# Kernel optimization log

Hardware: AMD Instinct MI355X
Metric: run time of the kernel (lower is better)

Reference implementation:

```python
import jax, jax.numpy as jnp
import numpy as np

GELU_C = 0.7978845608028654  # sqrt(2/pi)

def new_gelu(x):
    return 0.5 * x * (1.0 + jnp.tanh(GELU_C * (x + 0.044715 * x ** 3)))

def signed_quant(x, num_non_signbits, max_value):
    n = 2 ** num_non_signbits
    return jnp.sign(x) * jnp.minimum(jnp.round(jnp.abs(x) / max_value * n) + 1.0, float(n - 1))

def reverse_signed_quant(q, num_non_signbits, max_value):
    n = 2 ** num_non_signbits
    return jnp.sign(q) * (jnp.abs(q) - 1.0) / n * max_value

def setup_inputs() -> dict:
    key = jax.random.key(0)
    k1, k2, k3 = jax.random.split(key, 3)
    B, S, NX, NF = 4, 2048, 1024, 4096
    inp = jax.random.normal(k1, (B, S, NX), dtype=jnp.float32)
    weight = jax.random.normal(k2, (NX, NF), dtype=jnp.float32) * 0.02
    bias = jnp.zeros((NF,), dtype=jnp.float32)
    return {"input": inp, "weight": weight, "bias": bias}

def reference(input, weight, bias):
    # idx = 0 -> threshold=0.0, num_bits_to_calculate=3, weight bits=3
    threshold = 0.0
    num_bits = 3
    w_bits = 3
    max_input_value = 8.0
    nx = weight.shape[0]
    # per-input-row power-of-two weight scale: [nx, 1]
    max_weight_value = 2.0 ** jnp.round(jnp.log2(jnp.max(jnp.abs(weight), axis=-1, keepdims=True)))
    in_q = signed_quant(input, num_bits, max_input_value)
    w_q = signed_quant(weight, w_bits, max_weight_value)
    b_q = signed_quant(bias, num_bits, max_input_value)
    # low-precision prediction scores
    out_sign = (in_q @ w_q) / nx / (2.0 ** ((num_bits + w_bits) / 2))
    # dequantized approximate output + GELU
    out_rev = (reverse_signed_quant(in_q, num_bits, max_input_value)
               @ reverse_signed_quant(w_q, w_bits, max_weight_value)
               + reverse_signed_quant(b_q, num_bits, max_input_value))
    gelu_rev = new_gelu(out_rev)
    # full-precision path
    full = new_gelu(input @ weight + bias)
    return jnp.where(out_sign < threshold, gelu_rev, full)
```

## Files before the change

### kernel.cpp

```cpp
#include <hip/hip_runtime.h>
#include <hip/hip_bf16.h>

#define M_DIM 8192
#define K_DIM 1024
#define N_DIM 4096
#define BUF_BYTES 32768

typedef __attribute__((ext_vector_type(8))) short bf16x8;
typedef __attribute__((ext_vector_type(4))) int i32x4;
typedef __attribute__((ext_vector_type(16))) int i32x16;
typedef __attribute__((ext_vector_type(16))) float f32x16;

__device__ __forceinline__ short f2bf(float f) {
  unsigned u = __builtin_bit_cast(unsigned, f);
  u = (u + 0x7fffu + ((u >> 16) & 1u)) >> 16;
  return (short)u;
}

__device__ __forceinline__ unsigned f2fp8(float v) {
  unsigned b = __builtin_bit_cast(unsigned, v);
  unsigned sg = (b >> 24) & 0x80u;
  unsigned ab = b & 0x7fffffffu;
  if (ab == 0) return sg;
  int e = (int)(ab >> 23) - 127;
  unsigned m3 = (ab >> 20) & 7u;
  if (e >= -6) return sg | (unsigned)((e + 7) << 3) | m3;
  return sg | ((8u + m3) >> (-6 - e));
}

__device__ __forceinline__ float gelu_f(float x) {
  float u = 0.7978845608028654f * (x + 0.044715f * x * x * x);
  float e = __expf(2.0f * u);
  float t = 1.0f - 2.0f / (e + 1.0f);
  return 0.5f * x * (1.0f + t);
}

__device__ __forceinline__ void gload16(const void* g, void* l) {
  __builtin_amdgcn_global_load_lds((const __attribute__((address_space(1))) void*)g,
                                   (__attribute__((address_space(3))) void*)l, 16, 0, 0);
}

__global__ void rowmax_kernel(const float* __restrict__ w, float* __restrict__ mw) {
  int row = blockIdx.x * 4 + (threadIdx.x >> 6);
  int lane = threadIdx.x & 63;
  const float4* rp = (const float4*)(w + (size_t)row * N_DIM);
  float m = 0.0f;
#pragma unroll
  for (int it = 0; it < 16; ++it) {
    float4 v = rp[it * 64 + lane];
    m = fmaxf(m, fmaxf(fmaxf(fabsf(v.x), fabsf(v.y)), fmaxf(fabsf(v.z), fabsf(v.w))));
  }
#pragma unroll
  for (int off = 32; off > 0; off >>= 1) m = fmaxf(m, __shfl_xor(m, off, 64));
  if (lane == 0) mw[row] = exp2f(rintf(log2f(m)));
}

__global__ void prep_a_kernel(const float* __restrict__ inp, signed char* __restrict__ aqi,
                              unsigned char* __restrict__ adf, short* __restrict__ af) {
  int c = blockIdx.x * 256 + threadIdx.x;
  int kg = c >> 13, m = c & 8191;
  const float4* src = (const float4*)(inp + (size_t)m * K_DIM + kg * 16);
  float xs[16];
#pragma unroll
  for (int v = 0; v < 4; ++v) {
    float4 t = src[v];
    xs[v * 4 + 0] = t.x; xs[v * 4 + 1] = t.y; xs[v * 4 + 2] = t.z; xs[v * 4 + 3] = t.w;
  }
  int qi[4] = {0, 0, 0, 0};
  unsigned long long f8lo = 0ull, f8hi = 0ull;
  bf16x8 b0, b1;
#pragma unroll
  for (int j = 0; j < 16; ++j) {
    float x = xs[j];
    float s = (x > 0.f) ? 1.f : ((x < 0.f) ? -1.f : 0.f);
    float r = rintf(fabsf(x));
    int iq = (int)(s * fminf(r + 1.f, 7.f));
    qi[j >> 2] |= (iq & 255) << ((j & 3) * 8);
    unsigned f8 = f2fp8(s * fminf(r, 6.f));
    if (j < 8) f8lo |= (unsigned long long)f8 << (j * 8);
    else       f8hi |= (unsigned long long)f8 << ((j - 8) * 8);
    short bb = f2bf(x);
    if (j < 8) b0[j] = bb; else b1[j - 8] = bb;
  }
  *(i32x4*)(aqi + ((size_t)kg * M_DIM + m) * 16) = (i32x4){qi[0], qi[1], qi[2], qi[3]};
  *(unsigned long long*)(adf + ((size_t)(2 * kg) * M_DIM + m) * 8) = f8lo;
  *(unsigned long long*)(adf + ((size_t)(2 * kg + 1) * M_DIM + m) * 8) = f8hi;
  *(bf16x8*)(af + ((size_t)(2 * kg) * M_DIM + m) * 8) = b0;
  *(bf16x8*)(af + ((size_t)(2 * kg + 1) * M_DIM + m) * 8) = b1;
}

__global__ void prep_w_kernel(const float* __restrict__ w, const float* __restrict__ mw,
                              signed char* __restrict__ wqi, unsigned char* __restrict__ wdf,
                              short* __restrict__ wf) {
  int c = blockIdx.x * 256 + threadIdx.x;
  int kg = c >> 12, n = c & 4095;
  int qi[4] = {0, 0, 0, 0};
  unsigned long long f8lo = 0ull, f8hi = 0ull;
  bf16x8 b0, b1;
#pragma unroll
  for (int j = 0; j < 16; ++j) {
    float wv = w[(size_t)(kg * 16 + j) * N_DIM + n];
    float sc = mw[kg * 16 + j];
    float s = (wv > 0.f) ? 1.f : ((wv < 0.f) ? -1.f : 0.f);
    float r = rintf(fabsf(wv) * (8.0f / sc));
    int iq = (int)(s * fminf(r + 1.f, 7.f));
    qi[j >> 2] |= (iq & 255) << ((j & 3) * 8);
    unsigned f8 = f2fp8(s * fminf(r, 6.f) * 0.125f * sc);
    if (j < 8) f8lo |= (unsigned long long)f8 << (j * 8);
    else       f8hi |= (unsigned long long)f8 << ((j - 8) * 8);
    short bb = f2bf(wv);
    if (j < 8) b0[j] = bb; else b1[j - 8] = bb;
  }
  *(i32x4*)(wqi + ((size_t)kg * N_DIM + n) * 16) = (i32x4){qi[0], qi[1], qi[2], qi[3]};
  *(unsigned long long*)(wdf + ((size_t)(2 * kg) * N_DIM + n) * 8) = f8lo;
  *(unsigned long long*)(wdf + ((size_t)(2 * kg + 1) * N_DIM + n) * 8) = f8hi;
  *(bf16x8*)(wf + ((size_t)(2 * kg) * N_DIM + n) * 8) = b0;
  *(bf16x8*)(wf + ((size_t)(2 * kg + 1) * N_DIM + n) * 8) = b1;
}

__global__ __launch_bounds__(256, 2) void fused_gemm_kernel(
    const signed char* __restrict__ aqi, const unsigned char* __restrict__ adf,
    const short* __restrict__ af, const signed char* __restrict__ wqi,
    const unsigned char* __restrict__ wdf, const short* __restrict__ wf,
    const float* __restrict__ bias, float* __restrict__ out) {
  extern __shared__ char lds[];

  const int tid = threadIdx.x;
  const int wid = tid >> 6;
  const int lane = tid & 63;

  int bid = blockIdx.x;
  bid = (bid & 7) * 256 + (bid >> 3);
  const int bm0 = (bid >> 5) * 128;
  const int bn0 = (bid & 31) * 128;

  const int wr = wid >> 1;
  const int wc = wid & 1;

  const char* gb[8]; int gs[8]; int lo[8];
#pragma unroll
  for (int i = 0; i < 8; ++i) {
    int u = wid * 8 + i;
    lo[i] = u * 1024 + lane * 16;
    if (u < 4) {
      int o = u * 64 + lane; int h2 = o >> 7, row = o & 127;
      gb[i] = (const char*)aqi + ((size_t)h2 * M_DIM + bm0 + row) * 16;
      gs[i] = 32 * M_DIM;
    } else if (u < 8) {
      int kg = u - 4;
      gb[i] = (const char*)adf + ((size_t)kg * M_DIM + bm0) * 8 + lane * 16;
      gs[i] = 32 * M_DIM;
    } else if (u < 16) {
      int o = (u - 8) * 64 + lane; int kg = o >> 7, row = o & 127;
      gb[i] = (const char*)af + ((size_t)kg * M_DIM + bm0 + row) * 16;
      gs[i] = 64 * M_DIM;
    } else if (u < 20) {
      int o = (u - 16) * 64 + lane; int h2 = o >> 7, col = o & 127;
      gb[i] = (const char*)wqi + ((size_t)h2 * N_DIM + bn0 + col) * 16;
      gs[i] = 32 * N_DIM;
    } else if (u < 24) {
      int kg = u - 20;
      gb[i] = (const char*)wdf + ((size_t)kg * N_DIM + bn0) * 8 + lane * 16;
      gs[i] = 32 * N_DIM;
    } else {
      int o = (u - 24) * 64 + lane; int kg = o >> 7, col = o & 127;
      gb[i] = (const char*)wf + ((size_t)kg * N_DIM + bn0 + col) * 16;
      gs[i] = 64 * N_DIM;
    }
  }

  const int h = lane >> 5;
  const int l31 = lane & 31;
  const int ra = wr * 64 + l31;
  const int rb = wc * 64 + l31;

  i32x16 acc0[2][2];
  f32x16 acc1[2][2], acc2[2][2];
  const i32x16 zi = {0, 0, 0, 0, 0, 0, 0, 0, 0, 0, 0, 0, 0, 0, 0, 0};
  const f32x16 zf = {0, 0, 0, 0, 0, 0, 0, 0, 0, 0, 0, 0, 0, 0, 0, 0};
#pragma unroll
  for (int mf = 0; mf < 2; ++mf)
#pragma unroll
    for (int nf = 0; nf < 2; ++nf) { acc0[mf][nf] = zi; acc1[mf][nf] = zf; acc2[mf][nf] = zf; }

#pragma unroll
  for (int i = 0; i < 8; ++i) gload16(gb[i], lds + lo[i]);

  for (int t = 0; t < 32; ++t) {
    const int cb = (t & 1) * BUF_BYTES;
    if (t < 31) {
      const int nb = ((t + 1) & 1) * BUF_BYTES;
#pragma unroll
      for (int i = 0; i < 8; ++i)
        gload16(gb[i] + (size_t)(t + 1) * gs[i], lds + nb + lo[i]);
      asm volatile("s_waitcnt vmcnt(8)" ::: "memory");
    } else {
      asm volatile("s_waitcnt vmcnt(0)" ::: "memory");
    }
    __builtin_amdgcn_s_barrier();
    __builtin_amdgcn_sched_barrier(0);

    const char* B = lds + cb;
    __builtin_amdgcn_s_setprio(1);
    {
      i32x4 a0[2], b0[2];
#pragma unroll
      for (int mf = 0; mf < 2; ++mf)
        a0[mf] = *(const i32x4*)(B + (h * 128 + ra + mf * 32) * 16);
#pragma unroll
      for (int nf = 0; nf < 2; ++nf)
        b0[nf] = *(const i32x4*)(B + 16384 + (h * 128 + rb + nf * 32) * 16);
#pragma unroll
      for (int mf = 0; mf < 2; ++mf)
#pragma unroll
        for (int nf = 0; nf < 2; ++nf)
          acc0[mf][nf] =
              __builtin_amdgcn_mfma_i32_32x32x32_i8(a0[mf], b0[nf], acc0[mf][nf], 0, 0, 0);
    }
#pragma unroll
    for (int kk = 0; kk < 2; ++kk) {
      long a1[2], b1[2];
#pragma unroll
      for (int mf = 0; mf < 2; ++mf)
        a1[mf] = *(const long*)(B + 4096 + ((kk * 2 + h) * 128 + ra + mf * 32) * 8);
#pragma unroll
      for (int nf = 0; nf < 2; ++nf)
        b1[nf] = *(const long*)(B + 20480 + ((kk * 2 + h) * 128 + rb + nf * 32) * 8);
#pragma unroll
      for (int mf = 0; mf < 2; ++mf)
#pragma unroll
        for (int nf = 0; nf < 2; ++nf)
          acc1[mf][nf] = __builtin_amdgcn_mfma_f32_32x32x16_fp8_fp8(a1[mf], b1[nf],
                                                                    acc1[mf][nf], 0, 0, 0);
    }
#pragma unroll
    for (int kk = 0; kk < 2; ++kk) {
      bf16x8 a2[2], b2[2];
#pragma unroll
      for (int mf = 0; mf < 2; ++mf)
        a2[mf] = *(const bf16x8*)(B + 8192 + ((kk * 2 + h) * 128 + ra + mf * 32) * 16);
#pragma unroll
      for (int nf = 0; nf < 2; ++nf)
        b2[nf] = *(const bf16x8*)(B + 24576 + ((kk * 2 + h) * 128 + rb + nf * 32) * 16);
#pragma unroll
      for (int mf = 0; mf < 2; ++mf)
#pragma unroll
        for (int nf = 0; nf < 2; ++nf)
          acc2[mf][nf] = __builtin_amdgcn_mfma_f32_32x32x16_bf16(a2[mf], b2[nf],
                                                                 acc2[mf][nf], 0, 0, 0);
    }
    __builtin_amdgcn_s_setprio(0);
    asm volatile("s_waitcnt lgkmcnt(0)" ::: "memory");
    __builtin_amdgcn_sched_barrier(0);
    __builtin_amdgcn_s_barrier();
  }

#pragma unroll
  for (int nf = 0; nf < 2; ++nf) {
    const int col = bn0 + rb + nf * 32;
    const float bv = bias[col];
    const float sb = (bv > 0.f) ? 1.f : ((bv < 0.f) ? -1.f : 0.f);
    const float db = sb * fminf(rintf(fabsf(bv)), 6.f);
#pragma unroll
    for (int mf = 0; mf < 2; ++mf) {
#pragma unroll
      for (int r = 0; r < 16; ++r) {
        const int row = bm0 + wr * 64 + mf * 32 + (r & 3) + 8 * (r >> 2) + 4 * h;
        float x = (acc0[mf][nf][r] < 0) ? (acc1[mf][nf][r] + db) : (acc2[mf][nf][r] + bv);
        out[(size_t)row * N_DIM + col] = gelu_f(x);
      }
    }
  }
}

extern "C" void kernel_launch(void* const* d_in, const int* in_sizes, int n_in,
                              void* d_out, int out_size, void* d_ws, size_t ws_size,
                              hipStream_t stream) {
  const float* inp = (const float*)d_in[0];
  const float* w = (const float*)d_in[1];
  const float* bias = (const float*)d_in[2];
  float* out = (float*)d_out;

  char* p = (char*)d_ws;
  short* af = (short*)p;             p += (size_t)M_DIM * K_DIM * 2;
  short* wf = (short*)p;             p += (size_t)K_DIM * N_DIM * 2;
  signed char* aqi = (signed char*)p; p += (size_t)M_DIM * K_DIM;
  unsigned char* adf = (unsigned char*)p; p += (size_t)M_DIM * K_DIM;
  signed char* wqi = (signed char*)p; p += (size_t)K_DIM * N_DIM;
  unsigned char* wdf = (unsigned char*)p; p += (size_t)K_DIM * N_DIM;
  float* mw = (float*)p;

  const int lds_bytes = 2 * BUF_BYTES;
  hipFuncSetAttribute((const void*)fused_gemm_kernel,
                      hipFuncAttributeMaxDynamicSharedMemorySize, lds_bytes);

  rowmax_kernel<<<K_DIM / 4, 256, 0, stream>>>(w, mw);
  prep_a_kernel<<<(M_DIM * K_DIM / 16) / 256, 256, 0, stream>>>(inp, aqi, adf, af);
  prep_w_kernel<<<(K_DIM * N_DIM / 16) / 256, 256, 0, stream>>>(w, mw, wqi, wdf, wf);
  fused_gemm_kernel<<<(M_DIM / 128) * (N_DIM / 128), 256, lds_bytes, stream>>>(
      aqi, adf, af, wqi, wdf, wf, bias, out);
}
```

Measured before the change: 213.0 us.

## Reshape GEMM tiles to 256x64, stream weight fragments directly into registers

Changes the block tile from 128x128 to 256x64, with each of four waves owning 64 rows across all 64 columns. Only the activation operands are staged through LDS, with dedicated waves loading each stream. The weight fragments (int8, fp8, bf16) are loaded straight from global memory into registers, and the vmcnt waits are adjusted to match. The XCD-aware block mapping is rewritten for the new grid. The aim is to halve LDS traffic and drop the weight LDS reads, at the cost of uncoalesced, unshared global weight loads and lower reuse of the weight operand.

```diff
diff --git a/kernel.cpp b/kernel.cpp
--- a/kernel.cpp
+++ b/kernel.cpp
@@ -126,53 +126,18 @@
   extern __shared__ char lds[];
 
   const int tid = threadIdx.x;
-  const int wid = tid >> 6;
+  const int wid_s = __builtin_amdgcn_readfirstlane(tid >> 6);
   const int lane = tid & 63;
 
-  int bid = blockIdx.x;
-  bid = (bid & 7) * 256 + (bid >> 3);
-  const int bm0 = (bid >> 5) * 128;
-  const int bn0 = (bid & 31) * 128;
-
-  const int wr = wid >> 1;
-  const int wc = wid & 1;
-
-  const char* gb[8]; int gs[8]; int lo[8];
-#pragma unroll
-  for (int i = 0; i < 8; ++i) {
-    int u = wid * 8 + i;
-    lo[i] = u * 1024 + lane * 16;
-    if (u < 4) {
-      int o = u * 64 + lane; int h2 = o >> 7, row = o & 127;
-      gb[i] = (const char*)aqi + ((size_t)h2 * M_DIM + bm0 + row) * 16;
-      gs[i] = 32 * M_DIM;
-    } else if (u < 8) {
-      int kg = u - 4;
-      gb[i] = (const char*)adf + ((size_t)kg * M_DIM + bm0) * 8 + lane * 16;
-      gs[i] = 32 * M_DIM;
-    } else if (u < 16) {
-      int o = (u - 8) * 64 + lane; int kg = o >> 7, row = o & 127;
-      gb[i] = (const char*)af + ((size_t)kg * M_DIM + bm0 + row) * 16;
-      gs[i] = 64 * M_DIM;
-    } else if (u < 20) {
-      int o = (u - 16) * 64 + lane; int h2 = o >> 7, col = o & 127;
-      gb[i] = (const char*)wqi + ((size_t)h2 * N_DIM + bn0 + col) * 16;
-      gs[i] = 32 * N_DIM;
-    } else if (u < 24) {
-      int kg = u - 20;
-      gb[i] = (const char*)wdf + ((size_t)kg * N_DIM + bn0) * 8 + lane * 16;
-      gs[i] = 32 * N_DIM;
-    } else {
-      int o = (u - 24) * 64 + lane; int kg = o >> 7, col = o & 127;
-      gb[i] = (const char*)wf + ((size_t)kg * N_DIM + bn0 + col) * 16;
-      gs[i] = 64 * N_DIM;
-    }
-  }
+  int raw = blockIdx.x;
+  int xcd = raw & 7, local = raw >> 3;
+  const int bm0 = ((xcd >> 2) * 16 + (local >> 4)) * 256;
+  const int bn0 = ((xcd & 3) * 16 + (local & 15)) * 64;
 
   const int h = lane >> 5;
   const int l31 = lane & 31;
-  const int ra = wr * 64 + l31;
-  const int rb = wc * 64 + l31;
+  const int ra = wid_s * 64 + l31;
+  const int cb = bn0 + l31;
 
   i32x16 acc0[2][2];
   f32x16 acc1[2][2], acc2[2][2];
@@ -183,33 +148,72 @@
 #pragma unroll
     for (int nf = 0; nf < 2; ++nf) { acc0[mf][nf] = zi; acc1[mf][nf] = zf; acc2[mf][nf] = zf; }
 
-#pragma unroll
-  for (int i = 0; i < 8; ++i) gload16(gb[i], lds + lo[i]);
-
+  auto stage = [&](int t, char* buf) {
+    if (wid_s == 0) {
+#pragma unroll
+      for (int i = 0; i < 8; ++i)
+        gload16((const char*)aqi +
+                    ((size_t)(2 * t + (i >> 2)) * M_DIM + bm0 + (i & 3) * 64 + lane) * 16,
+                buf + i * 1024 + lane * 16);
+    } else if (wid_s == 1) {
+#pragma unroll
+      for (int i = 0; i < 8; ++i)
+        gload16((const char*)adf + ((size_t)(4 * t + (i >> 1)) * M_DIM + bm0 + (i & 1) * 128) * 8 +
+                    lane * 16,
+                buf + (8 + i) * 1024 + lane * 16);
+    } else {
+#pragma unroll
+      for (int i = 0; i < 8; ++i) {
+        int j = (wid_s - 2) * 8 + i;
+        gload16((const char*)af +
+                    ((size_t)(4 * t + (j >> 2)) * M_DIM + bm0 + (j & 3) * 64 + lane) * 16,
+                buf + (16 + j) * 1024 + lane * 16);
+      }
+    }
+  };
+
+  const char* pq0 = (const char*)wqi + ((size_t)h * N_DIM + cb) * 16;
+  const char* pq1 = (const char*)wdf + ((size_t)h * N_DIM + cb) * 8;
+  const char* pq2 = (const char*)wf + ((size_t)h * N_DIM + cb) * 16;
+  const size_t sq0 = (size_t)2 * N_DIM * 16;
+  const size_t sq1 = (size_t)4 * N_DIM * 8;
+  const size_t sq2 = (size_t)4 * N_DIM * 16;
+  const size_t kq1 = (size_t)2 * N_DIM * 8;
+  const size_t kq2 = (size_t)2 * N_DIM * 16;
+
+  stage(0, lds);
+
+#pragma unroll 1
   for (int t = 0; t < 32; ++t) {
-    const int cb = (t & 1) * BUF_BYTES;
-    if (t < 31) {
-      const int nb = ((t + 1) & 1) * BUF_BYTES;
-#pragma unroll
-      for (int i = 0; i < 8; ++i)
-        gload16(gb[i] + (size_t)(t + 1) * gs[i], lds + nb + lo[i]);
-      asm volatile("s_waitcnt vmcnt(8)" ::: "memory");
-    } else {
-      asm volatile("s_waitcnt vmcnt(0)" ::: "memory");
-    }
+    char* Bb = lds + (t & 1) * BUF_BYTES;
+    if (t < 31) stage(t + 1, lds + ((t + 1) & 1) * BUF_BYTES);
+
+    i32x4 b0[2]; long b1[2][2]; bf16x8 b2[2][2];
+#pragma unroll
+    for (int nf = 0; nf < 2; ++nf) b0[nf] = *(const i32x4*)(pq0 + nf * 512);
+#pragma unroll
+    for (int kk = 0; kk < 2; ++kk)
+#pragma unroll
+      for (int nf = 0; nf < 2; ++nf) b1[kk][nf] = *(const long*)(pq1 + kk * kq1 + nf * 256);
+#pragma unroll
+    for (int kk = 0; kk < 2; ++kk)
+#pragma unroll
+      for (int nf = 0; nf < 2; ++nf) b2[kk][nf] = *(const bf16x8*)(pq2 + kk * kq2 + nf * 512);
+    pq0 += sq0; pq1 += sq1; pq2 += sq2;
+
+    if (t < 31)
+      asm volatile("s_waitcnt vmcnt(18)" ::: "memory");
+    else
+      asm volatile("s_waitcnt vmcnt(10)" ::: "memory");
     __builtin_amdgcn_s_barrier();
     __builtin_amdgcn_sched_barrier(0);
 
-    const char* B = lds + cb;
     __builtin_amdgcn_s_setprio(1);
     {
-      i32x4 a0[2], b0[2];
-#pragma unroll
-      for (int mf = 0; mf < 2; ++mf)
-        a0[mf] = *(const i32x4*)(B + (h * 128 + ra + mf * 32) * 16);
-#pragma unroll
-      for (int nf = 0; nf < 2; ++nf)
-        b0[nf] = *(const i32x4*)(B + 16384 + (h * 128 + rb + nf * 32) * 16);
+      i32x4 a0[2];
+#pragma unroll
+      for (int mf = 0; mf < 2; ++mf)
+        a0[mf] = *(const i32x4*)(Bb + (h * 256 + ra + mf * 32) * 16);
 #pragma unroll
       for (int mf = 0; mf < 2; ++mf)
 #pragma unroll
@@ -219,34 +223,28 @@
     }
 #pragma unroll
     for (int kk = 0; kk < 2; ++kk) {
-      long a1[2], b1[2];
-#pragma unroll
-      for (int mf = 0; mf < 2; ++mf)
-        a1[mf] = *(const long*)(B + 4096 + ((kk * 2 + h) * 128 + ra + mf * 32) * 8);
-#pragma unroll
-      for (int nf = 0; nf < 2; ++nf)
-        b1[nf] = *(const long*)(B + 20480 + ((kk * 2 + h) * 128 + rb + nf * 32) * 8);
+      long a1[2];
+#pragma unroll
+      for (int mf = 0; mf < 2; ++mf)
+        a1[mf] = *(const long*)(Bb + 8192 + ((kk * 2 + h) * 256 + ra + mf * 32) * 8);
 #pragma unroll
       for (int mf = 0; mf < 2; ++mf)
 #pragma unroll
         for (int nf = 0; nf < 2; ++nf)
-          acc1[mf][nf] = __builtin_amdgcn_mfma_f32_32x32x16_fp8_fp8(a1[mf], b1[nf],
+          acc1[mf][nf] = __builtin_amdgcn_mfma_f32_32x32x16_fp8_fp8(a1[mf], b1[kk][nf],
                                                                     acc1[mf][nf], 0, 0, 0);
     }
 #pragma unroll
     for (int kk = 0; kk < 2; ++kk) {
-      bf16x8 a2[2], b2[2];
-#pragma unroll
-      for (int mf = 0; mf < 2; ++mf)
-        a2[mf] = *(const bf16x8*)(B + 8192 + ((kk * 2 + h) * 128 + ra + mf * 32) * 16);
-#pragma unroll
-      for (int nf = 0; nf < 2; ++nf)
-        b2[nf] = *(const bf16x8*)(B + 24576 + ((kk * 2 + h) * 128 + rb + nf * 32) * 16);
+      bf16x8 a2[2];
+#pragma unroll
+      for (int mf = 0; mf < 2; ++mf)
+        a2[mf] = *(const bf16x8*)(Bb + 16384 + ((kk * 2 + h) * 256 + ra + mf * 32) * 16);
 #pragma unroll
       for (int mf = 0; mf < 2; ++mf)
 #pragma unroll
         for (int nf = 0; nf < 2; ++nf)
-          acc2[mf][nf] = __builtin_amdgcn_mfma_f32_32x32x16_bf16(a2[mf], b2[nf],
+          acc2[mf][nf] = __builtin_amdgcn_mfma_f32_32x32x16_bf16(a2[mf], b2[kk][nf],
                                                                  acc2[mf][nf], 0, 0, 0);
     }
     __builtin_amdgcn_s_setprio(0);
@@ -257,7 +255,7 @@
 
 #pragma unroll
   for (int nf = 0; nf < 2; ++nf) {
-    const int col = bn0 + rb + nf * 32;
+    const int col = cb + nf * 32;
     const float bv = bias[col];
     const float sb = (bv > 0.f) ? 1.f : ((bv < 0.f) ? -1.f : 0.f);
     const float db = sb * fminf(rintf(fabsf(bv)), 6.f);
@@ -265,7 +263,7 @@
     for (int mf = 0; mf < 2; ++mf) {
 #pragma unroll
       for (int r = 0; r < 16; ++r) {
-        const int row = bm0 + wr * 64 + mf * 32 + (r & 3) + 8 * (r >> 2) + 4 * h;
+        const int row = bm0 + wid_s * 64 + mf * 32 + (r & 3) + 8 * (r >> 2) + 4 * h;
         float x = (acc0[mf][nf][r] < 0) ? (acc1[mf][nf][r] + db) : (acc2[mf][nf][r] + bv);
         out[(size_t)row * N_DIM + col] = gelu_f(x);
       }
@@ -297,6 +295,6 @@
   rowmax_kernel<<<K_DIM / 4, 256, 0, stream>>>(w, mw);
   prep_a_kernel<<<(M_DIM * K_DIM / 16) / 256, 256, 0, stream>>>(inp, aqi, adf, af);
   prep_w_kernel<<<(K_DIM * N_DIM / 16) / 256, 256, 0, stream>>>(w, mw, wqi, wdf, wf);
-  fused_gemm_kernel<<<(M_DIM / 128) * (N_DIM / 128), 256, lds_bytes, stream>>>(
+  fused_gemm_kernel<<<(M_DIM / 256) * (N_DIM / 64), 256, lds_bytes, stream>>>(
       aqi, adf, af, wqi, wdf, wf, bias, out);
 }
```

After: 246.6 us. 15.8% more time.

## Split fused GEMM into selector kernel and full bf16 kernel with bitmask

Applied to the files above, without the earlier changes.

Splits the three-GEMM fused kernel in two. The first kernel computes the int8 sign GEMM and the fp8 GEMM, now using the scaled f8f6f4 MFMA at K=64 with a 16-byte packed fp8 layout. It writes the negative-branch outputs and a per-element selection bitmask. The second kernel runs the bf16 GEMM with a larger 128x256 tile and writes only the elements the mask leaves unselected, trading an extra launch and bitmask traffic for better per-kernel tiling and fewer fp8 MFMA instructions.

```diff
diff --git a/kernel.cpp b/kernel.cpp
--- a/kernel.cpp
+++ b/kernel.cpp
@@ -4,10 +4,10 @@
 #define M_DIM 8192
 #define K_DIM 1024
 #define N_DIM 4096
-#define BUF_BYTES 32768
 
 typedef __attribute__((ext_vector_type(8))) short bf16x8;
 typedef __attribute__((ext_vector_type(4))) int i32x4;
+typedef __attribute__((ext_vector_type(8))) int i32x8;
 typedef __attribute__((ext_vector_type(16))) int i32x16;
 typedef __attribute__((ext_vector_type(16))) float f32x16;
 
@@ -67,7 +67,7 @@
     xs[v * 4 + 0] = t.x; xs[v * 4 + 1] = t.y; xs[v * 4 + 2] = t.z; xs[v * 4 + 3] = t.w;
   }
   int qi[4] = {0, 0, 0, 0};
-  unsigned long long f8lo = 0ull, f8hi = 0ull;
+  int qf[4] = {0, 0, 0, 0};
   bf16x8 b0, b1;
 #pragma unroll
   for (int j = 0; j < 16; ++j) {
@@ -77,14 +77,12 @@
     int iq = (int)(s * fminf(r + 1.f, 7.f));
     qi[j >> 2] |= (iq & 255) << ((j & 3) * 8);
     unsigned f8 = f2fp8(s * fminf(r, 6.f));
-    if (j < 8) f8lo |= (unsigned long long)f8 << (j * 8);
-    else       f8hi |= (unsigned long long)f8 << ((j - 8) * 8);
+    qf[j >> 2] |= (int)f8 << ((j & 3) * 8);
     short bb = f2bf(x);
     if (j < 8) b0[j] = bb; else b1[j - 8] = bb;
   }
   *(i32x4*)(aqi + ((size_t)kg * M_DIM + m) * 16) = (i32x4){qi[0], qi[1], qi[2], qi[3]};
-  *(unsigned long long*)(adf + ((size_t)(2 * kg) * M_DIM + m) * 8) = f8lo;
-  *(unsigned long long*)(adf + ((size_t)(2 * kg + 1) * M_DIM + m) * 8) = f8hi;
+  *(i32x4*)(adf + ((size_t)kg * M_DIM + m) * 16) = (i32x4){qf[0], qf[1], qf[2], qf[3]};
   *(bf16x8*)(af + ((size_t)(2 * kg) * M_DIM + m) * 8) = b0;
   *(bf16x8*)(af + ((size_t)(2 * kg + 1) * M_DIM + m) * 8) = b1;
 }
@@ -95,7 +93,7 @@
   int c = blockIdx.x * 256 + threadIdx.x;
   int kg = c >> 12, n = c & 4095;
   int qi[4] = {0, 0, 0, 0};
-  unsigned long long f8lo = 0ull, f8hi = 0ull;
+  int qf[4] = {0, 0, 0, 0};
   bf16x8 b0, b1;
 #pragma unroll
   for (int j = 0; j < 16; ++j) {
@@ -106,25 +104,23 @@
     int iq = (int)(s * fminf(r + 1.f, 7.f));
     qi[j >> 2] |= (iq & 255) << ((j & 3) * 8);
     unsigned f8 = f2fp8(s * fminf(r, 6.f) * 0.125f * sc);
-    if (j < 8) f8lo |= (unsigned long long)f8 << (j * 8);
-    else       f8hi |= (unsigned long long)f8 << ((j - 8) * 8);
+    qf[j >> 2] |= (int)f8 << ((j & 3) * 8);
     short bb = f2bf(wv);
     if (j < 8) b0[j] = bb; else b1[j - 8] = bb;
   }
   *(i32x4*)(wqi + ((size_t)kg * N_DIM + n) * 16) = (i32x4){qi[0], qi[1], qi[2], qi[3]};
-  *(unsigned long long*)(wdf + ((size_t)(2 * kg) * N_DIM + n) * 8) = f8lo;
-  *(unsigned long long*)(wdf + ((size_t)(2 * kg + 1) * N_DIM + n) * 8) = f8hi;
+  *(i32x4*)(wdf + ((size_t)kg * N_DIM + n) * 16) = (i32x4){qf[0], qf[1], qf[2], qf[3]};
   *(bf16x8*)(wf + ((size_t)(2 * kg) * N_DIM + n) * 8) = b0;
   *(bf16x8*)(wf + ((size_t)(2 * kg + 1) * N_DIM + n) * 8) = b1;
 }
 
-__global__ __launch_bounds__(256, 2) void fused_gemm_kernel(
+#define S_BUF 32768
+__global__ __launch_bounds__(256, 2) void sel_kernel(
     const signed char* __restrict__ aqi, const unsigned char* __restrict__ adf,
-    const short* __restrict__ af, const signed char* __restrict__ wqi,
-    const unsigned char* __restrict__ wdf, const short* __restrict__ wf,
-    const float* __restrict__ bias, float* __restrict__ out) {
+    const signed char* __restrict__ wqi, const unsigned char* __restrict__ wdf,
+    const float* __restrict__ bias, unsigned int* __restrict__ bmask,
+    float* __restrict__ out) {
   extern __shared__ char lds[];
-
   const int tid = threadIdx.x;
   const int wid = tid >> 6;
   const int lane = tid & 63;
@@ -134,65 +130,52 @@
   const int bm0 = (bid >> 5) * 128;
   const int bn0 = (bid & 31) * 128;
 
-  const int wr = wid >> 1;
-  const int wc = wid & 1;
-
-  const char* gb[8]; int gs[8]; int lo[8];
+  const int wr = wid >> 1, wc = wid & 1;
+  const int h = lane >> 5, l31 = lane & 31;
+  const int ra = wr * 64 + l31;
+  const int rb = wc * 64 + l31;
+
+  i32x16 acc0[2][2];
+  f32x16 acc1[2][2];
+  const i32x16 zi = {0, 0, 0, 0, 0, 0, 0, 0, 0, 0, 0, 0, 0, 0, 0, 0};
+  const f32x16 zf = {0, 0, 0, 0, 0, 0, 0, 0, 0, 0, 0, 0, 0, 0, 0, 0};
+#pragma unroll
+  for (int mf = 0; mf < 2; ++mf)
+#pragma unroll
+    for (int nf = 0; nf < 2; ++nf) { acc0[mf][nf] = zi; acc1[mf][nf] = zf; }
+
+  const char* gb[8]; int lo[8]; int gs[8];
 #pragma unroll
   for (int i = 0; i < 8; ++i) {
     int u = wid * 8 + i;
     lo[i] = u * 1024 + lane * 16;
-    if (u < 4) {
-      int o = u * 64 + lane; int h2 = o >> 7, row = o & 127;
-      gb[i] = (const char*)aqi + ((size_t)h2 * M_DIM + bm0 + row) * 16;
-      gs[i] = 32 * M_DIM;
-    } else if (u < 8) {
-      int kg = u - 4;
-      gb[i] = (const char*)adf + ((size_t)kg * M_DIM + bm0) * 8 + lane * 16;
-      gs[i] = 32 * M_DIM;
+    if (u < 8) {
+      gb[i] = (const char*)aqi + ((size_t)(u >> 1) * M_DIM + bm0 + (u & 1) * 64 + lane) * 16;
+      gs[i] = 4 * M_DIM * 16;
     } else if (u < 16) {
-      int o = (u - 8) * 64 + lane; int kg = o >> 7, row = o & 127;
-      gb[i] = (const char*)af + ((size_t)kg * M_DIM + bm0 + row) * 16;
-      gs[i] = 64 * M_DIM;
-    } else if (u < 20) {
-      int o = (u - 16) * 64 + lane; int h2 = o >> 7, col = o & 127;
-      gb[i] = (const char*)wqi + ((size_t)h2 * N_DIM + bn0 + col) * 16;
-      gs[i] = 32 * N_DIM;
+      int v = u - 8;
+      gb[i] = (const char*)adf + ((size_t)(v >> 1) * M_DIM + bm0 + (v & 1) * 64 + lane) * 16;
+      gs[i] = 4 * M_DIM * 16;
     } else if (u < 24) {
-      int kg = u - 20;
-      gb[i] = (const char*)wdf + ((size_t)kg * N_DIM + bn0) * 8 + lane * 16;
-      gs[i] = 32 * N_DIM;
+      int v = u - 16;
+      gb[i] = (const char*)wqi + ((size_t)(v >> 1) * N_DIM + bn0 + (v & 1) * 64 + lane) * 16;
+      gs[i] = 4 * N_DIM * 16;
     } else {
-      int o = (u - 24) * 64 + lane; int kg = o >> 7, col = o & 127;
-      gb[i] = (const char*)wf + ((size_t)kg * N_DIM + bn0 + col) * 16;
-      gs[i] = 64 * N_DIM;
-    }
-  }
-
-  const int h = lane >> 5;
-  const int l31 = lane & 31;
-  const int ra = wr * 64 + l31;
-  const int rb = wc * 64 + l31;
-
-  i32x16 acc0[2][2];
-  f32x16 acc1[2][2], acc2[2][2];
-  const i32x16 zi = {0, 0, 0, 0, 0, 0, 0, 0, 0, 0, 0, 0, 0, 0, 0, 0};
-  const f32x16 zf = {0, 0, 0, 0, 0, 0, 0, 0, 0, 0, 0, 0, 0, 0, 0, 0};
-#pragma unroll
-  for (int mf = 0; mf < 2; ++mf)
-#pragma unroll
-    for (int nf = 0; nf < 2; ++nf) { acc0[mf][nf] = zi; acc1[mf][nf] = zf; acc2[mf][nf] = zf; }
+      int v = u - 24;
+      gb[i] = (const char*)wdf + ((size_t)(v >> 1) * N_DIM + bn0 + (v & 1) * 64 + lane) * 16;
+      gs[i] = 4 * N_DIM * 16;
+    }
+  }
 
 #pragma unroll
   for (int i = 0; i < 8; ++i) gload16(gb[i], lds + lo[i]);
 
-  for (int t = 0; t < 32; ++t) {
-    const int cb = (t & 1) * BUF_BYTES;
-    if (t < 31) {
-      const int nb = ((t + 1) & 1) * BUF_BYTES;
-#pragma unroll
-      for (int i = 0; i < 8; ++i)
-        gload16(gb[i] + (size_t)(t + 1) * gs[i], lds + nb + lo[i]);
+  for (int t = 0; t < 16; ++t) {
+    const char* Bb = lds + (t & 1) * S_BUF;
+    if (t < 15) {
+      char* nb = lds + ((t + 1) & 1) * S_BUF;
+#pragma unroll
+      for (int i = 0; i < 8; ++i) gload16(gb[i] + (size_t)(t + 1) * gs[i], nb + lo[i]);
       asm volatile("s_waitcnt vmcnt(8)" ::: "memory");
     } else {
       asm volatile("s_waitcnt vmcnt(0)" ::: "memory");
@@ -200,16 +183,16 @@
     __builtin_amdgcn_s_barrier();
     __builtin_amdgcn_sched_barrier(0);
 
-    const char* B = lds + cb;
     __builtin_amdgcn_s_setprio(1);
-    {
+#pragma unroll
+    for (int kk = 0; kk < 2; ++kk) {
       i32x4 a0[2], b0[2];
 #pragma unroll
       for (int mf = 0; mf < 2; ++mf)
-        a0[mf] = *(const i32x4*)(B + (h * 128 + ra + mf * 32) * 16);
+        a0[mf] = *(const i32x4*)(Bb + ((kk * 2 + h) * 128 + ra + mf * 32) * 16);
 #pragma unroll
       for (int nf = 0; nf < 2; ++nf)
-        b0[nf] = *(const i32x4*)(B + 16384 + (h * 128 + rb + nf * 32) * 16);
+        b0[nf] = *(const i32x4*)(Bb + 16384 + ((kk * 2 + h) * 128 + rb + nf * 32) * 16);
 #pragma unroll
       for (int mf = 0; mf < 2; ++mf)
 #pragma unroll
@@ -217,37 +200,28 @@
           acc0[mf][nf] =
               __builtin_amdgcn_mfma_i32_32x32x32_i8(a0[mf], b0[nf], acc0[mf][nf], 0, 0, 0);
     }
-#pragma unroll
-    for (int kk = 0; kk < 2; ++kk) {
-      long a1[2], b1[2];
+    {
+      i32x8 a1[2], b1[2];
+#pragma unroll
+      for (int mf = 0; mf < 2; ++mf) {
+        i32x4 plo = *(const i32x4*)(Bb + 8192 + ((h * 2 + 0) * 128 + ra + mf * 32) * 16);
+        i32x4 phi = *(const i32x4*)(Bb + 8192 + ((h * 2 + 1) * 128 + ra + mf * 32) * 16);
+#pragma unroll
+        for (int j = 0; j < 4; ++j) { a1[mf][j] = plo[j]; a1[mf][4 + j] = phi[j]; }
+      }
+#pragma unroll
+      for (int nf = 0; nf < 2; ++nf) {
+        i32x4 plo = *(const i32x4*)(Bb + 24576 + ((h * 2 + 0) * 128 + rb + nf * 32) * 16);
+        i32x4 phi = *(const i32x4*)(Bb + 24576 + ((h * 2 + 1) * 128 + rb + nf * 32) * 16);
+#pragma unroll
+        for (int j = 0; j < 4; ++j) { b1[nf][j] = plo[j]; b1[nf][4 + j] = phi[j]; }
+      }
 #pragma unroll
       for (int mf = 0; mf < 2; ++mf)
-        a1[mf] = *(const long*)(B + 4096 + ((kk * 2 + h) * 128 + ra + mf * 32) * 8);
-#pragma unroll
-      for (int nf = 0; nf < 2; ++nf)
-        b1[nf] = *(const long*)(B + 20480 + ((kk * 2 + h) * 128 + rb + nf * 32) * 8);
-#pragma unroll
-      for (int mf = 0; mf < 2; ++mf)
 #pragma unroll
         for (int nf = 0; nf < 2; ++nf)
-          acc1[mf][nf] = __builtin_amdgcn_mfma_f32_32x32x16_fp8_fp8(a1[mf], b1[nf],
-                                                                    acc1[mf][nf], 0, 0, 0);
-    }
-#pragma unroll
-    for (int kk = 0; kk < 2; ++kk) {
-      bf16x8 a2[2], b2[2];
-#pragma unroll
-      for (int mf = 0; mf < 2; ++mf)
-        a2[mf] = *(const bf16x8*)(B + 8192 + ((kk * 2 + h) * 128 + ra + mf * 32) * 16);
-#pragma unroll
-      for (int nf = 0; nf < 2; ++nf)
-        b2[nf] = *(const bf16x8*)(B + 24576 + ((kk * 2 + h) * 128 + rb + nf * 32) * 16);
-#pragma unroll
-      for (int mf = 0; mf < 2; ++mf)
-#pragma unroll
-        for (int nf = 0; nf < 2; ++nf)
-          acc2[mf][nf] = __builtin_amdgcn_mfma_f32_32x32x16_bf16(a2[mf], b2[nf],
-                                                                 acc2[mf][nf], 0, 0, 0);
+          acc1[mf][nf] = __builtin_amdgcn_mfma_scale_f32_32x32x64_f8f6f4(
+              a1[mf], b1[nf], acc1[mf][nf], 0, 0, 0, 0x7f7f7f7f, 0, 0x7f7f7f7f);
     }
     __builtin_amdgcn_s_setprio(0);
     asm volatile("s_waitcnt lgkmcnt(0)" ::: "memory");
@@ -258,6 +232,7 @@
 #pragma unroll
   for (int nf = 0; nf < 2; ++nf) {
     const int col = bn0 + rb + nf * 32;
+    const int cw = col >> 5;
     const float bv = bias[col];
     const float sb = (bv > 0.f) ? 1.f : ((bv < 0.f) ? -1.f : 0.f);
     const float db = sb * fminf(rintf(fabsf(bv)), 6.f);
@@ -265,9 +240,110 @@
     for (int mf = 0; mf < 2; ++mf) {
 #pragma unroll
       for (int r = 0; r < 16; ++r) {
-        const int row = bm0 + wr * 64 + mf * 32 + (r & 3) + 8 * (r >> 2) + 4 * h;
-        float x = (acc0[mf][nf][r] < 0) ? (acc1[mf][nf][r] + db) : (acc2[mf][nf][r] + bv);
-        out[(size_t)row * N_DIM + col] = gelu_f(x);
+        const int row0 = bm0 + wr * 64 + mf * 32 + (r & 3) + 8 * (r >> 2);
+        const int row = row0 + 4 * h;
+        bool sel = acc0[mf][nf][r] < 0;
+        unsigned long long b = __ballot((int)sel);
+        if (lane == 0) bmask[(size_t)row0 * 128 + cw] = (unsigned int)b;
+        if (lane == 32) bmask[(size_t)(row0 + 4) * 128 + cw] = (unsigned int)(b >> 32);
+        if (sel) out[(size_t)row * N_DIM + col] = gelu_f(acc1[mf][nf][r] + db);
+      }
+    }
+  }
+}
+
+#define F_BUF 24576
+__global__ __launch_bounds__(256, 2) void full_kernel(
+    const short* __restrict__ af, const short* __restrict__ wf,
+    const float* __restrict__ bias, const unsigned int* __restrict__ bmask,
+    float* __restrict__ out) {
+  extern __shared__ char lds[];
+  const int tid = threadIdx.x;
+  const int wid = tid >> 6;
+  const int lane = tid & 63;
+
+  int bid = blockIdx.x;
+  bid = (bid & 7) * 128 + (bid >> 3);
+  const int bm0 = (bid >> 4) * 128;
+  const int bn0 = (bid & 15) * 256;
+
+  const int h = lane >> 5, l31 = lane & 31;
+
+  f32x16 acc[4][2];
+  const f32x16 zf = {0, 0, 0, 0, 0, 0, 0, 0, 0, 0, 0, 0, 0, 0, 0, 0};
+#pragma unroll
+  for (int mf = 0; mf < 4; ++mf)
+#pragma unroll
+    for (int nf = 0; nf < 2; ++nf) acc[mf][nf] = zf;
+
+  const char* gb[6]; int lo[6]; int gs[6];
+#pragma unroll
+  for (int i = 0; i < 6; ++i) {
+    int u = wid * 6 + i;
+    lo[i] = u * 1024 + lane * 16;
+    if (u < 8) {
+      gb[i] = (const char*)af + ((size_t)(u >> 1) * M_DIM + bm0 + (u & 1) * 64 + lane) * 16;
+      gs[i] = 4 * M_DIM * 16;
+    } else {
+      int v = u - 8;
+      gb[i] = (const char*)wf + ((size_t)(v >> 2) * N_DIM + bn0 + (v & 3) * 64 + lane) * 16;
+      gs[i] = 4 * N_DIM * 16;
+    }
+  }
+
+#pragma unroll
+  for (int i = 0; i < 6; ++i) gload16(gb[i], lds + lo[i]);
+
+  for (int t = 0; t < 32; ++t) {
+    const char* Bb = lds + (t & 1) * F_BUF;
+    if (t < 31) {
+      char* nb = lds + ((t + 1) & 1) * F_BUF;
+#pragma unroll
+      for (int i = 0; i < 6; ++i) gload16(gb[i] + (size_t)(t + 1) * gs[i], nb + lo[i]);
+      asm volatile("s_waitcnt vmcnt(6)" ::: "memory");
+    } else {
+      asm volatile("s_waitcnt vmcnt(0)" ::: "memory");
+    }
+    __builtin_amdgcn_s_barrier();
+    __builtin_amdgcn_sched_barrier(0);
+
+    __builtin_amdgcn_s_setprio(1);
+#pragma unroll
+    for (int kk = 0; kk < 2; ++kk) {
+      bf16x8 a2[4], b2[2];
+#pragma unroll
+      for (int mf = 0; mf < 4; ++mf)
+        a2[mf] = *(const bf16x8*)(Bb + ((kk * 2 + h) * 128 + mf * 32 + l31) * 16);
+#pragma unroll
+      for (int nf = 0; nf < 2; ++nf)
+        b2[nf] = *(const bf16x8*)(Bb + 8192 +
+                                  ((kk * 2 + h) * 256 + wid * 64 + nf * 32 + l31) * 16);
+#pragma unroll
+      for (int mf = 0; mf < 4; ++mf)
+#pragma unroll
+        for (int nf = 0; nf < 2; ++nf)
+          acc[mf][nf] =
+              __builtin_amdgcn_mfma_f32_32x32x16_bf16(a2[mf], b2[nf], acc[mf][nf], 0, 0, 0);
+    }
+    __builtin_amdgcn_s_setprio(0);
+    asm volatile("s_waitcnt lgkmcnt(0)" ::: "memory");
+    __builtin_amdgcn_sched_barrier(0);
+    __builtin_amdgcn_s_barrier();
+  }
+
+#pragma unroll
+  for (int nf = 0; nf < 2; ++nf) {
+    const int col = bn0 + wid * 64 + nf * 32 + l31;
+    const int cw = col >> 5;
+    const float bv = bias[col];
+#pragma unroll
+    for (int mf = 0; mf < 4; ++mf) {
+#pragma unroll
+      for (int r = 0; r < 16; ++r) {
+        const int row = bm0 + mf * 32 + (r & 3) + 8 * (r >> 2) + 4 * h;
+        unsigned int wsel = bmask[(size_t)row * 128 + cw];
+        if (!((wsel >> (col & 31)) & 1u))
+          out[(size_t)row * N_DIM + col] = gelu_f(acc[mf][nf][r] + bv);
       }
     }
   }
@@ -282,21 +358,25 @@
   float* out = (float*)d_out;
 
   char* p = (char*)d_ws;
-  short* af = (short*)p;             p += (size_t)M_DIM * K_DIM * 2;
-  short* wf = (short*)p;             p += (size_t)K_DIM * N_DIM * 2;
-  signed char* aqi = (signed char*)p; p += (size_t)M_DIM * K_DIM;
+  short* af = (short*)p;                  p += (size_t)M_DIM * K_DIM * 2;
+  short* wf = (short*)p;                  p += (size_t)K_DIM * N_DIM * 2;
+  signed char* aqi = (signed char*)p;     p += (size_t)M_DIM * K_DIM;
   unsigned char* adf = (unsigned char*)p; p += (size_t)M_DIM * K_DIM;
-  signed char* wqi = (signed char*)p; p += (size_t)K_DIM * N_DIM;
+  signed char* wqi = (signed char*)p;     p += (size_t)K_DIM * N_DIM;
   unsigned char* wdf = (unsigned char*)p; p += (size_t)K_DIM * N_DIM;
+  unsigned int* bmask = (unsigned int*)p; p += (size_t)M_DIM * N_DIM / 8;
   float* mw = (float*)p;
 
-  const int lds_bytes = 2 * BUF_BYTES;
-  hipFuncSetAttribute((const void*)fused_gemm_kernel,
-                      hipFuncAttributeMaxDynamicSharedMemorySize, lds_bytes);
+  hipFuncSetAttribute((const void*)sel_kernel,
+                      hipFuncAttributeMaxDynamicSharedMemorySize, 2 * S_BUF);
+  hipFuncSetAttribute((const void*)full_kernel,
+                      hipFuncAttributeMaxDynamicSharedMemorySize, 2 * F_BUF);
 
   rowmax_kernel<<<K_DIM / 4, 256, 0, stream>>>(w, mw);
   prep_a_kernel<<<(M_DIM * K_DIM / 16) / 256, 256, 0, stream>>>(inp, aqi, adf, af);
   prep_w_kernel<<<(K_DIM * N_DIM / 16) / 256, 256, 0, stream>>>(w, mw, wqi, wdf, wf);
-  fused_gemm_kernel<<<(M_DIM / 128) * (N_DIM / 128), 256, lds_bytes, stream>>>(
-      aqi, adf, af, wqi, wdf, wf, bias, out);
-}
+  sel_kernel<<<(M_DIM / 128) * (N_DIM / 128), 256, 2 * S_BUF, stream>>>(
+      aqi, adf, wqi, wdf, bias, bmask, out);
+  full_kernel<<<(M_DIM / 128) * (N_DIM / 256), 256, 2 * F_BUF, stream>>>(
+      af, wf, bias, bmask, out);
+}
```

After: 340.1 us. 59.7% more time.
